# Optimization experiments

Measured on AMD Instinct MI355X. Metric: run time of the kernel, lower is better.

The kernel has to match this reference:

```python
import jax, jax.numpy as jnp
import numpy as np

IN_F, OUT_F, LAT, RES, K, B = 512, 512, 512, 64, 3, 8
EPS = 1e-08
C_LIN = 1.0 / np.sqrt(LAT)          # EqualizedWeight scale for linear
C_CONV = 1.0 / np.sqrt(IN_F * K * K)  # EqualizedWeight scale for conv


def setup_inputs() -> dict:
    key = jax.random.key(0)
    k1, k2, k3, k4 = jax.random.split(key, 4)
    return {
        "x": jax.random.normal(k1, (B, IN_F, RES, RES), dtype=jnp.float32),
        "latent": jax.random.normal(k2, (B, LAT), dtype=jnp.float32),
        "w_lin": jax.random.normal(k3, (IN_F, LAT), dtype=jnp.float32),
        "b_lin": jnp.ones((IN_F,), dtype=jnp.float32),
        "w_conv": jax.random.normal(k4, (OUT_F, IN_F, K, K), dtype=jnp.float32),
        "b_conv": jnp.zeros((OUT_F,), dtype=jnp.float32),
    }


def reference(x, latent, w_lin, b_lin, w_conv, b_conv):
    # EqualizedLinear: s = latent @ (w_lin*c).T + b_lin*lr_mul  -> [B, IN_F]
    s = latent @ (w_lin * C_LIN).T + b_lin
    # ModulatedConv2d. Per-sample weight w[b,o,i,k,k] = (w_conv*c)[o,i,k,k]*s[b,i],
    # demodulated by sigma_inv[b,o] = rsqrt(sum_{i,k,k} w^2 + eps).
    w = w_conv * C_CONV  # [O, I, K, K]
    # sum_{k,k} w^2 over spatial -> [O, I], then contract with s^2 -> [B, O]
    w2 = jnp.sum(w * w, axis=(2, 3))  # [O, I]
    sigma_inv = jax.lax.rsqrt(jnp.einsum('oi,bi->bo', w2, s * s) + EPS)
    # conv(x, w*s_b) == conv(x * s_b, w): modulate input, single batched conv,
    # then demodulate output per (b, o). Avoids materializing B*O filters.
    x_mod = x * s[:, :, None, None]
    y = jax.lax.conv_general_dilated(
        x_mod, w,
        window_strides=(1, 1),
        padding=[((K - 1) // 2, (K - 1) // 2)] * 2,
        dimension_numbers=('NCHW', 'OIHW', 'NCHW'),
    )
    y = y * sigma_inv[:, :, None, None] + b_conv[None, :, None, None]
    return y
```

## Files before the change

### kernel.cpp

```cpp
#include <hip/hip_runtime.h>
#include <hip/hip_bf16.h>

#define IN_F 512
#define OUT_F 512
#define LATD 512
#define RES 64
#define BATCH 8
#define EPSV 1e-8f

static constexpr float C_LIN  = 0.04419417382415922f;
static constexpr float C_CONV = 0.014731391274719739f;

typedef __attribute__((ext_vector_type(8)))  short short8;
typedef __attribute__((ext_vector_type(16))) float f32x16;

union BF { __hip_bfloat16 h; short s; };

__device__ __forceinline__ void async_load16(const char* g, char* l) {
  __builtin_amdgcn_global_load_lds(
      (const __attribute__((address_space(1))) unsigned int*)g,
      (__attribute__((address_space(3))) unsigned int*)l, 16, 0, 0);
}

__global__ void k_compute_s(const float* __restrict__ latent,
                            const float* __restrict__ w_lin,
                            const float* __restrict__ b_lin,
                            float* __restrict__ s) {
  const int i = blockIdx.x;
  const int lane = threadIdx.x;
  const float4* wl = (const float4*)(w_lin + (size_t)i * LATD);
  const float4 w0 = wl[lane * 2], w1 = wl[lane * 2 + 1];
  float acc[BATCH];
#pragma unroll
  for (int b = 0; b < BATCH; ++b) {
    const float4* lt = (const float4*)(latent + (size_t)b * LATD);
    const float4 l0 = lt[lane * 2], l1 = lt[lane * 2 + 1];
    acc[b] = w0.x * l0.x + w0.y * l0.y + w0.z * l0.z + w0.w * l0.w +
             w1.x * l1.x + w1.y * l1.y + w1.z * l1.z + w1.w * l1.w;
  }
#pragma unroll
  for (int b = 0; b < BATCH; ++b) {
    float v = acc[b];
#pragma unroll
    for (int off = 32; off > 0; off >>= 1) v += __shfl_down(v, off);
    if (lane == 0) s[b * IN_F + i] = v * C_LIN + b_lin[i];
  }
}

__global__ void k_prep_w(const float* __restrict__ w_conv,
                         short* __restrict__ wb,
                         float* __restrict__ w2) {
  const int t = blockIdx.x * 256 + threadIdx.x;
  const int o = t >> 9;
  const int i = t & 511;
  const float* src = w_conv + (size_t)t * 9;
  const int c = i >> 4, ob = o >> 6, ol = o & 63, i16 = i & 15;
  float sum = 0.f;
#pragma unroll
  for (int tap = 0; tap < 9; ++tap) {
    const float v = src[tap] * C_CONV;
    sum += v * v;
    BF cv; cv.h = __float2bfloat16(v);
    wb[(size_t)((c * 8 + ob) * 9 + tap) * 1024 + ol * 16 + i16] = cv.s;
  }
  w2[t] = sum;
}

__global__ void k_sigma(const float* __restrict__ w2,
                        const float* __restrict__ s,
                        float* __restrict__ sigma_inv) {
  const int o = blockIdx.x * 4 + (threadIdx.x >> 6);
  const int lane = threadIdx.x & 63;
  float acc[BATCH];
#pragma unroll
  for (int b = 0; b < BATCH; ++b) acc[b] = 0.f;
#pragma unroll
  for (int k = 0; k < 8; ++k) {
    const int i = k * 64 + lane;
    const float w = w2[o * IN_F + i];
#pragma unroll
    for (int b = 0; b < BATCH; ++b) {
      const float sv = s[b * IN_F + i];
      acc[b] += w * sv * sv;
    }
  }
#pragma unroll
  for (int b = 0; b < BATCH; ++b) {
    float v = acc[b];
#pragma unroll
    for (int off = 32; off > 0; off >>= 1) v += __shfl_down(v, off);
    if (lane == 0) sigma_inv[b * OUT_F + o] = rsqrtf(v + EPSV);
  }
}

__global__ void k_zero_border(char* __restrict__ xmp) {
  char* base = xmp + (size_t)blockIdx.x * 139392;
  for (int q = threadIdx.x; q < 520; q += 256) {
    const int cell = q >> 1, half = q & 1;
    int hp, wp;
    if (cell < 66)       { hp = 0;              wp = cell; }
    else if (cell < 132) { hp = 65;             wp = cell - 66; }
    else if (cell < 196) { hp = cell - 132 + 1; wp = 0; }
    else                 { hp = cell - 196 + 1; wp = 65; }
    *(uint4*)(base + ((size_t)hp * 66 + wp) * 32 + half * 16) = make_uint4(0u, 0u, 0u, 0u);
  }
}

__global__ void k_modulate(const float* __restrict__ x,
                           const float* __restrict__ s,
                           char* __restrict__ xmp) {
  const int h    = blockIdx.x & 63;
  const int ic32 = (blockIdx.x >> 6) & 15;
  const int b    = blockIdx.x >> 10;
  __shared__ float tile[32][65];
  const int tid = threadIdx.x;
  {
    const int il = tid >> 3, w8 = (tid & 7) * 8;
    const int i = ic32 * 32 + il;
    const float sv = s[b * IN_F + i];
    const float* xp = x + (((size_t)(b * IN_F + i) * RES + h) * RES + w8);
    const float4 v0 = *(const float4*)xp;
    const float4 v1 = *(const float4*)(xp + 4);
    tile[il][w8 + 0] = v0.x * sv; tile[il][w8 + 1] = v0.y * sv;
    tile[il][w8 + 2] = v0.z * sv; tile[il][w8 + 3] = v0.w * sv;
    tile[il][w8 + 4] = v1.x * sv; tile[il][w8 + 5] = v1.y * sv;
    tile[il][w8 + 6] = v1.z * sv; tile[il][w8 + 7] = v1.w * sv;
  }
  __syncthreads();
  {
    const int w = tid >> 2, part = tid & 3;
    const int chalf = part >> 1, half = part & 1;
    short8 pk;
#pragma unroll
    for (int j = 0; j < 8; ++j) {
      BF cv; cv.h = __float2bfloat16(tile[chalf * 16 + half * 8 + j][w]);
      pk[j] = cv.s;
    }
    const int c = ic32 * 2 + chalf;
    char* dst = xmp + (size_t)(c * 8 + b) * 139392 +
                ((size_t)(h + 1) * 66 + (w + 1)) * 32 + half * 16;
    *(short8*)dst = pk;
  }
}

__global__ __launch_bounds__(256, 2)
void k_conv(const char* __restrict__ xmp,
            const short* __restrict__ wbg,
            const float* __restrict__ sigma_inv,
            const float* __restrict__ b_conv,
            float* __restrict__ out) {
  __shared__ __align__(16) char lds[79104];
  const int ob = blockIdx.x;
  const int o0 = ob * 64;
  const int b  = blockIdx.y >> 3;
  const int h0 = (blockIdx.y & 7) * 8;
  const int tid = threadIdx.x;
  const int wave = tid >> 6, lane = tid & 63;
  const int l31 = lane & 31, half = lane >> 5;

  f32x16 acc[2][4];
#pragma unroll
  for (int i = 0; i < 2; ++i)
#pragma unroll
    for (int j = 0; j < 4; ++j)
#pragma unroll
      for (int r = 0; r < 16; ++r) acc[i][j][r] = 0.f;

  const char* xsrc0 = xmp + (size_t)b * 139392 + (size_t)h0 * 2112;
  const char* wsrc0 = (const char*)wbg + (size_t)ob * 18432;

#pragma unroll
  for (int k = 0; k < 5; ++k) {
    const int j = tid + k * 256;
    async_load16(xsrc0 + j * 16, lds + j * 16);
  }
  if (tid < 40) { const int j = 1280 + tid; async_load16(xsrc0 + j * 16, lds + j * 16); }
#pragma unroll
  for (int k = 0; k < 4; ++k) {
    const int j = tid + k * 256;
    async_load16(wsrc0 + j * 16, lds + 42240 + j * 16);
  }
  if (tid < 128) { const int j = 1024 + tid; async_load16(wsrc0 + j * 16, lds + 42240 + j * 16); }
  __syncthreads();

  for (int ic = 0; ic < 32; ++ic) {
    const int p = ic & 1;
    if (ic + 1 < 32) {
      const char* xs = xsrc0 + (size_t)(ic + 1) * (8 * 139392);
      const char* wsr = wsrc0 + (size_t)(ic + 1) * (8 * 18432);
      char* xd = lds + (p ^ 1) * 21120;
      char* wd = lds + 42240 + (p ^ 1) * 18432;
#pragma unroll
      for (int k = 0; k < 5; ++k) {
        const int j = tid + k * 256;
        async_load16(xs + j * 16, xd + j * 16);
      }
      if (tid < 40) { const int j = 1280 + tid; async_load16(xs + j * 16, xd + j * 16); }
#pragma unroll
      for (int k = 0; k < 4; ++k) {
        const int j = tid + k * 256;
        async_load16(wsr + j * 16, wd + j * 16);
      }
      if (tid < 128) { const int j = 1024 + tid; async_load16(wsr + j * 16, wd + j * 16); }
    }
    const char* xp = lds + p * 21120;
    const char* wp = lds + 42240 + p * 18432;
#pragma unroll
    for (int tap = 0; tap < 9; ++tap) {
      const int dh = tap / 3, dw = tap - dh * 3;
      const short8 a0 = *(const short8*)(wp + (tap * 64 + l31) * 32 + half * 16);
      const short8 a1 = *(const short8*)(wp + (tap * 64 + 32 + l31) * 32 + half * 16);
#pragma unroll
      for (int tp = 0; tp < 4; ++tp) {
        const int hr = wave * 2 + (tp >> 1) + dh;
        const int wc = (tp & 1) * 32 + dw + l31;
        const short8 bf = *(const short8*)(xp + (hr * 66 + wc) * 32 + half * 16);
        acc[0][tp] = __builtin_amdgcn_mfma_f32_32x32x16_bf16(a0, bf, acc[0][tp], 0, 0, 0);
        acc[1][tp] = __builtin_amdgcn_mfma_f32_32x32x16_bf16(a1, bf, acc[1][tp], 0, 0, 0);
      }
    }
    __syncthreads();
  }

#pragma unroll
  for (int t_o = 0; t_o < 2; ++t_o) {
#pragma unroll
    for (int g = 0; g < 4; ++g) {
#pragma unroll
      for (int r = 0; r < 4; ++r) {
        const int o = o0 + t_o * 32 + r + 8 * g + 4 * half;
        const float sig  = sigma_inv[b * OUT_F + o];
        const float bias = b_conv[o];
        const int reg = g * 4 + r;
#pragma unroll
        for (int tp = 0; tp < 4; ++tp) {
          const int h = h0 + wave * 2 + (tp >> 1);
          const int w = (tp & 1) * 32 + l31;
          out[(((size_t)(b * OUT_F + o) * RES + h) * RES) + w] =
              acc[t_o][tp][reg] * sig + bias;
        }
      }
    }
  }
}

extern "C" void kernel_launch(void* const* d_in, const int* in_sizes, int n_in,
                              void* d_out, int out_size, void* d_ws, size_t ws_size,
                              hipStream_t stream) {
  const float* x      = (const float*)d_in[0];
  const float* latent = (const float*)d_in[1];
  const float* w_lin  = (const float*)d_in[2];
  const float* b_lin  = (const float*)d_in[3];
  const float* w_conv = (const float*)d_in[4];
  const float* b_conv = (const float*)d_in[5];
  float* out = (float*)d_out;

  char* ws = (char*)d_ws;
  char*  xmp       = ws;
  short* wb        = (short*)(ws + 35684352);
  float* w2        = (float*)(ws + 40402944);
  float* s         = (float*)(ws + 41451520);
  float* sigma_inv = (float*)(ws + 41467904);

  k_compute_s<<<IN_F, 64, 0, stream>>>(latent, w_lin, b_lin, s);
  k_prep_w<<<1024, 256, 0, stream>>>(w_conv, wb, w2);
  k_sigma<<<128, 256, 0, stream>>>(w2, s, sigma_inv);
  k_zero_border<<<256, 256, 0, stream>>>(xmp);
  k_modulate<<<BATCH * 16 * RES, 256, 0, stream>>>(x, s, xmp);
  dim3 grid(OUT_F / 64, BATCH * 8);
  k_conv<<<grid, 256, 0, stream>>>(xmp, wb, sigma_inv, b_conv, out);
}
```

Before: 253.0 us.

## Split channel halves in LDS layouts, fold border zeroing, reorder conv grid

Reorganizes the padded input and weight layouts so each 8-channel half occupies a contiguous 16-byte-stride plane, so MFMA operand reads from LDS are contiguous per lane group and should hit fewer bank conflicts. Border zeroing moves into the modulate kernel, removing one launch. The conv grid is flattened so blocks sharing an output-channel tile launch together, improving weight reuse in L2. k_compute_s is also packed four rows per block.

```diff
diff --git a/kernel.cpp b/kernel.cpp
--- a/kernel.cpp
+++ b/kernel.cpp
@@ -11,6 +11,8 @@
 static constexpr float C_LIN  = 0.04419417382415922f;
 static constexpr float C_CONV = 0.014731391274719739f;
 
+#define PLANE 139392
+
 typedef __attribute__((ext_vector_type(8)))  short short8;
 typedef __attribute__((ext_vector_type(16))) float f32x16;
 
@@ -26,8 +28,8 @@
                             const float* __restrict__ w_lin,
                             const float* __restrict__ b_lin,
                             float* __restrict__ s) {
-  const int i = blockIdx.x;
-  const int lane = threadIdx.x;
+  const int i = blockIdx.x * 4 + (threadIdx.x >> 6);
+  const int lane = threadIdx.x & 63;
   const float4* wl = (const float4*)(w_lin + (size_t)i * LATD);
   const float4 w0 = wl[lane * 2], w1 = wl[lane * 2 + 1];
   float acc[BATCH];
@@ -54,14 +56,15 @@
   const int o = t >> 9;
   const int i = t & 511;
   const float* src = w_conv + (size_t)t * 9;
-  const int c = i >> 4, ob = o >> 6, ol = o & 63, i16 = i & 15;
+  const int c = i >> 4, u = (i >> 3) & 1, i8 = i & 7;
+  const int ob = o >> 6, ol = o & 63;
   float sum = 0.f;
 #pragma unroll
   for (int tap = 0; tap < 9; ++tap) {
     const float v = src[tap] * C_CONV;
     sum += v * v;
     BF cv; cv.h = __float2bfloat16(v);
-    wb[(size_t)((c * 8 + ob) * 9 + tap) * 1024 + ol * 16 + i16] = cv.s;
+    wb[((((size_t)(c * 8 + ob) * 9 + tap) * 2 + u) * 64 + ol) * 8 + i8] = cv.s;
   }
   w2[t] = sum;
 }
@@ -90,19 +93,6 @@
 #pragma unroll
     for (int off = 32; off > 0; off >>= 1) v += __shfl_down(v, off);
     if (lane == 0) sigma_inv[b * OUT_F + o] = rsqrtf(v + EPSV);
-  }
-}
-
-__global__ void k_zero_border(char* __restrict__ xmp) {
-  char* base = xmp + (size_t)blockIdx.x * 139392;
-  for (int q = threadIdx.x; q < 520; q += 256) {
-    const int cell = q >> 1, half = q & 1;
-    int hp, wp;
-    if (cell < 66)       { hp = 0;              wp = cell; }
-    else if (cell < 132) { hp = 65;             wp = cell - 66; }
-    else if (cell < 196) { hp = cell - 132 + 1; wp = 0; }
-    else                 { hp = cell - 196 + 1; wp = 65; }
-    *(uint4*)(base + ((size_t)hp * 66 + wp) * 32 + half * 16) = make_uint4(0u, 0u, 0u, 0u);
   }
 }
 
@@ -128,18 +118,33 @@
   }
   __syncthreads();
   {
-    const int w = tid >> 2, part = tid & 3;
-    const int chalf = part >> 1, half = part & 1;
+    const int chalf = tid >> 7, u = (tid >> 6) & 1, w = tid & 63;
     short8 pk;
 #pragma unroll
     for (int j = 0; j < 8; ++j) {
-      BF cv; cv.h = __float2bfloat16(tile[chalf * 16 + half * 8 + j][w]);
+      BF cv; cv.h = __float2bfloat16(tile[chalf * 16 + u * 8 + j][w]);
       pk[j] = cv.s;
     }
     const int c = ic32 * 2 + chalf;
-    char* dst = xmp + (size_t)(c * 8 + b) * 139392 +
-                ((size_t)(h + 1) * 66 + (w + 1)) * 32 + half * 16;
+    char* dst = xmp + (size_t)(c * 8 + b) * PLANE +
+                ((size_t)(h + 1) * 132 + u * 66 + (w + 1)) * 16;
     *(short8*)dst = pk;
+  }
+  const uint4 z = make_uint4(0u, 0u, 0u, 0u);
+  if (tid < 8) {
+    const int chalf = tid & 1, u = (tid >> 1) & 1, wsel = tid >> 2;
+    char* dst = xmp + (size_t)((ic32 * 2 + chalf) * 8 + b) * PLANE +
+                ((size_t)(h + 1) * 132 + u * 66 + (wsel ? 65 : 0)) * 16;
+    *(uint4*)dst = z;
+  }
+  if (h == 0 || h == 63) {
+    const int row = (h == 0) ? 0 : 65;
+    for (int idx = tid; idx < 264; idx += 256) {
+      const int chalf = idx / 132, uu = idx - chalf * 132;
+      char* dst = xmp + (size_t)((ic32 * 2 + chalf) * 8 + b) * PLANE +
+                  ((size_t)row * 132 + uu) * 16;
+      *(uint4*)dst = z;
+    }
   }
 }
 
@@ -150,10 +155,12 @@
             const float* __restrict__ b_conv,
             float* __restrict__ out) {
   __shared__ __align__(16) char lds[79104];
-  const int ob = blockIdx.x;
+  const int bid = blockIdx.x;
+  const int g = bid & 63;
+  const int ob = bid >> 6;
   const int o0 = ob * 64;
-  const int b  = blockIdx.y >> 3;
-  const int h0 = (blockIdx.y & 7) * 8;
+  const int b  = g >> 3;
+  const int h0 = (g & 7) * 8;
   const int tid = threadIdx.x;
   const int wave = tid >> 6, lane = tid & 63;
   const int l31 = lane & 31, half = lane >> 5;
@@ -166,7 +173,7 @@
 #pragma unroll
       for (int r = 0; r < 16; ++r) acc[i][j][r] = 0.f;
 
-  const char* xsrc0 = xmp + (size_t)b * 139392 + (size_t)h0 * 2112;
+  const char* xsrc0 = xmp + (size_t)b * PLANE + (size_t)h0 * 2112;
   const char* wsrc0 = (const char*)wbg + (size_t)ob * 18432;
 
 #pragma unroll
@@ -186,7 +193,7 @@
   for (int ic = 0; ic < 32; ++ic) {
     const int p = ic & 1;
     if (ic + 1 < 32) {
-      const char* xs = xsrc0 + (size_t)(ic + 1) * (8 * 139392);
+      const char* xs  = xsrc0 + (size_t)(ic + 1) * (8 * PLANE);
       const char* wsr = wsrc0 + (size_t)(ic + 1) * (8 * 18432);
       char* xd = lds + (p ^ 1) * 21120;
       char* wd = lds + 42240 + (p ^ 1) * 18432;
@@ -208,13 +215,13 @@
 #pragma unroll
     for (int tap = 0; tap < 9; ++tap) {
       const int dh = tap / 3, dw = tap - dh * 3;
-      const short8 a0 = *(const short8*)(wp + (tap * 64 + l31) * 32 + half * 16);
-      const short8 a1 = *(const short8*)(wp + (tap * 64 + 32 + l31) * 32 + half * 16);
+      const short8 a0 = *(const short8*)(wp + (tap * 128 + half * 64 + l31) * 16);
+      const short8 a1 = *(const short8*)(wp + (tap * 128 + half * 64 + 32 + l31) * 16);
 #pragma unroll
       for (int tp = 0; tp < 4; ++tp) {
         const int hr = wave * 2 + (tp >> 1) + dh;
-        const int wc = (tp & 1) * 32 + dw + l31;
-        const short8 bf = *(const short8*)(xp + (hr * 66 + wc) * 32 + half * 16);
+        const int px = (tp & 1) * 32 + dw + l31;
+        const short8 bf = *(const short8*)(xp + ((size_t)hr * 132 + half * 66 + px) * 16);
         acc[0][tp] = __builtin_amdgcn_mfma_f32_32x32x16_bf16(a0, bf, acc[0][tp], 0, 0, 0);
         acc[1][tp] = __builtin_amdgcn_mfma_f32_32x32x16_bf16(a1, bf, acc[1][tp], 0, 0, 0);
       }
@@ -225,13 +232,13 @@
 #pragma unroll
   for (int t_o = 0; t_o < 2; ++t_o) {
 #pragma unroll
-    for (int g = 0; g < 4; ++g) {
+    for (int gg = 0; gg < 4; ++gg) {
 #pragma unroll
       for (int r = 0; r < 4; ++r) {
-        const int o = o0 + t_o * 32 + r + 8 * g + 4 * half;
+        const int o = o0 + t_o * 32 + r + 8 * gg + 4 * half;
         const float sig  = sigma_inv[b * OUT_F + o];
         const float bias = b_conv[o];
-        const int reg = g * 4 + r;
+        const int reg = gg * 4 + r;
 #pragma unroll
         for (int tp = 0; tp < 4; ++tp) {
           const int h = h0 + wave * 2 + (tp >> 1);
@@ -262,11 +269,9 @@
   float* s         = (float*)(ws + 41451520);
   float* sigma_inv = (float*)(ws + 41467904);
 
-  k_compute_s<<<IN_F, 64, 0, stream>>>(latent, w_lin, b_lin, s);
+  k_compute_s<<<IN_F / 4, 256, 0, stream>>>(latent, w_lin, b_lin, s);
   k_prep_w<<<1024, 256, 0, stream>>>(w_conv, wb, w2);
   k_sigma<<<128, 256, 0, stream>>>(w2, s, sigma_inv);
-  k_zero_border<<<256, 256, 0, stream>>>(xmp);
   k_modulate<<<BATCH * 16 * RES, 256, 0, stream>>>(x, s, xmp);
-  dim3 grid(OUT_F / 64, BATCH * 8);
-  k_conv<<<grid, 256, 0, stream>>>(xmp, wb, sigma_inv, b_conv, out);
-}
+  k_conv<<<512, 256, 0, stream>>>(xmp, wb, sigma_inv, b_conv, out);
+}
```

Result: no change. 253.9 us (+0.4%).
